# Kernel tuning notes

Measured on AMD Instinct MI355X. Metric: run time of the kernel, lower is better.

Reference implementation:

```python
import jax, jax.numpy as jnp
import numpy as np

NUM_BINS = 256
EPS = 1e-08


def setup_inputs() -> dict:
    key = jax.random.key(0)
    k1, k2 = jax.random.split(key)
    B, C, H, W = 16, 3, 512, 512
    pred = jax.random.uniform(k1, (B, C, H, W), dtype=jnp.float32)
    target = jax.random.uniform(k2, (B, C, H, W), dtype=jnp.float32)
    return {"pred": pred, "target": target}


def _compute_histogram(x):
    """Per-(batch, channel) 256-bin histogram of values in [0, 1].

    Faithful to torch.histc(bins=N, min=0, max=1): bin width 1/N,
    value v -> bin floor(v*N), with v == 1.0 landing in the last bin
    (handled by the clip). Values outside [0,1] are ignored.
    Implemented as a single fused scatter-add over all B*C histograms.
    """
    B, C, H, W = x.shape
    in_range = (x >= 0.0) & (x <= 1.0)
    bins = jnp.clip(jnp.floor(x * NUM_BINS).astype(jnp.int32), 0, NUM_BINS - 1)
    # flat index into [B*C, NUM_BINS] histogram array
    bc = jnp.arange(B * C, dtype=jnp.int32)[:, None]  # [B*C, 1]
    flat_idx = (bc * NUM_BINS + bins.reshape(B * C, H * W)).reshape(-1)
    weights = in_range.reshape(-1).astype(x.dtype)
    hist = jnp.zeros(B * C * NUM_BINS, dtype=x.dtype).at[flat_idx].add(weights)
    return hist.reshape(B, C, NUM_BINS)


def reference(pred, target):
    pred_hist = _compute_histogram(pred)
    target_hist = _compute_histogram(target)
    pred_hist = pred_hist / (pred_hist.sum(axis=2, keepdims=True) + EPS)
    target_hist = target_hist / (target_hist.sum(axis=2, keepdims=True) + EPS)
    return jnp.mean((pred_hist - target_hist) ** 2)
```

## Files before the change

kernel.cpp:

```cpp
#include <hip/hip_runtime.h>

#define NUM_BINS 256
#define PLANES 48
#define PLANE_ELEMS (512 * 512)
#define BPP 16
#define THREADS 256
#define F4_PER_BLOCK (PLANE_ELEMS / 4 / BPP)
#define F4_PER_THREAD (F4_PER_BLOCK / THREADS)
#define NSUB 8
#define HSTRIDE 257
#define BATCH 4

__global__ __launch_bounds__(THREADS) void hist_kernel(const float* __restrict__ pred,
                                                       const float* __restrict__ target,
                                                       unsigned* __restrict__ hist,
                                                       unsigned* __restrict__ totals) {
    __shared__ alignas(16) unsigned lh[NSUB * HSTRIDE];
    __shared__ unsigned twave[4];
    const int t = threadIdx.x;
    const int lane = t & 63;

    uint4* l4 = reinterpret_cast<uint4*>(lh);
    for (int i = t; i < (NSUB * HSTRIDE + 3) / 4; i += THREADS) l4[i] = make_uint4(0, 0, 0, 0);
    __syncthreads();

    const int gid   = blockIdx.x;
    const int which = gid / (PLANES * BPP);
    const int rem   = gid - which * (PLANES * BPP);
    const int plane = rem / BPP;
    const int cblk  = rem - plane * BPP;

    const float* src = which ? target : pred;
    const float4* p = reinterpret_cast<const float4*>(src + (size_t)plane * PLANE_ELEMS)
                      + (size_t)cblk * F4_PER_BLOCK;
    unsigned* gh = hist + (size_t)(which * PLANES + plane) * NUM_BINS;
    unsigned* tp = &totals[which * PLANES + plane];

    unsigned* sub = lh + (size_t)(lane & (NSUB - 1)) * HSTRIDE;

    float4 cur[BATCH], nxt[BATCH];
#pragma unroll
    for (int j = 0; j < BATCH; ++j) cur[j] = p[j * THREADS + t];

    for (int c = 0; c < F4_PER_THREAD / BATCH; ++c) {
        if (c + 1 < F4_PER_THREAD / BATCH) {
#pragma unroll
            for (int j = 0; j < BATCH; ++j)
                nxt[j] = p[(c + 1) * BATCH * THREADS + j * THREADS + t];
        }
#pragma unroll
        for (int j = 0; j < BATCH; ++j) {
            float e[4] = {cur[j].x, cur[j].y, cur[j].z, cur[j].w};
#pragma unroll
            for (int k = 0; k < 4; ++k) {
                int b = (int)(e[k] * 256.0f);
                b = b > 255 ? 255 : b;
                atomicAdd(&sub[b], 1u);
            }
        }
#pragma unroll
        for (int j = 0; j < BATCH; ++j) cur[j] = nxt[j];
    }
    __syncthreads();

    unsigned c = 0;
#pragma unroll
    for (int h = 0; h < NSUB; ++h) c += lh[h * HSTRIDE + t];
    if (c) atomicAdd(&gh[t], c);

    unsigned bt = c;
    for (int off = 32; off; off >>= 1) bt += __shfl_down(bt, off, 64);
    if ((t & 63) == 0) twave[t >> 6] = bt;
    __syncthreads();
    if (t == 0) atomicAdd(tp, twave[0] + twave[1] + twave[2] + twave[3]);
}

__global__ __launch_bounds__(1024) void loss_kernel(const unsigned* __restrict__ hist,
                                                    const unsigned* __restrict__ totals,
                                                    float* __restrict__ out) {
    __shared__ double inv[2 * PLANES];
    __shared__ double sd[16];
    const int t = threadIdx.x;
    if (t < 2 * PLANES) inv[t] = 1.0 / ((double)totals[t] + 1e-8);
    __syncthreads();

    const uint4* h4 = reinterpret_cast<const uint4*>(hist);
    double acc = 0.0;
    for (int i = t; i < (PLANES * NUM_BINS) / 4; i += 1024) {
        uint4 hp = h4[i];
        uint4 ht = h4[i + (PLANES * NUM_BINS) / 4];
        const double ip = inv[i >> 6];
        const double it = inv[PLANES + (i >> 6)];
        double d0 = (double)hp.x * ip - (double)ht.x * it;
        double d1 = (double)hp.y * ip - (double)ht.y * it;
        double d2 = (double)hp.z * ip - (double)ht.z * it;
        double d3 = (double)hp.w * ip - (double)ht.w * it;
        acc += d0 * d0 + d1 * d1 + d2 * d2 + d3 * d3;
    }
    for (int off = 32; off; off >>= 1) acc += __shfl_down(acc, off, 64);
    if ((t & 63) == 0) sd[t >> 6] = acc;
    __syncthreads();
    if (t == 0) {
        double s = 0.0;
        for (int w = 0; w < 16; ++w) s += sd[w];
        out[0] = (float)(s / (double)(PLANES * NUM_BINS));
    }
}

extern "C" void kernel_launch(void* const* d_in, const int* in_sizes, int n_in,
                              void* d_out, int out_size, void* d_ws, size_t ws_size,
                              hipStream_t stream) {
    const float* pred   = (const float*)d_in[0];
    const float* target = (const float*)d_in[1];
    float* out = (float*)d_out;
    unsigned* hist   = (unsigned*)d_ws;
    unsigned* totals = hist + (size_t)2 * PLANES * NUM_BINS;

    hipMemsetAsync(d_ws, 0, ((size_t)2 * PLANES * NUM_BINS + 2 * PLANES) * sizeof(unsigned), stream);
    hist_kernel<<<2 * PLANES * BPP, THREADS, 0, stream>>>(pred, target, hist, totals);
    loss_kernel<<<1, 1024, 0, stream>>>(hist, totals, out);
}
```

Baseline: 30.04 us.

## Replace global atomics and memset with per-block partial histograms and staged reductions

Each histogram block now writes its 256-bin partial histogram to its own workspace slot instead of atomically adding into shared global histograms and totals. This removes the memset launch and the global atomics. A per-plane kernel sums the 16 partials, computes the normalisation totals itself, and emits a per-plane loss, and a tiny final kernel reduces the 48 plane losses. The change trades the memset for one extra kernel launch and more workspace traffic for the partials.

```diff
diff --git a/kernel.cpp b/kernel.cpp
--- a/kernel.cpp
+++ b/kernel.cpp
@@ -13,10 +13,8 @@
 
 __global__ __launch_bounds__(THREADS) void hist_kernel(const float* __restrict__ pred,
                                                        const float* __restrict__ target,
-                                                       unsigned* __restrict__ hist,
-                                                       unsigned* __restrict__ totals) {
+                                                       unsigned* __restrict__ part) {
     __shared__ alignas(16) unsigned lh[NSUB * HSTRIDE];
-    __shared__ unsigned twave[4];
     const int t = threadIdx.x;
     const int lane = t & 63;
 
@@ -33,8 +31,6 @@
     const float* src = which ? target : pred;
     const float4* p = reinterpret_cast<const float4*>(src + (size_t)plane * PLANE_ELEMS)
                       + (size_t)cblk * F4_PER_BLOCK;
-    unsigned* gh = hist + (size_t)(which * PLANES + plane) * NUM_BINS;
-    unsigned* tp = &totals[which * PLANES + plane];
 
     unsigned* sub = lh + (size_t)(lane & (NSUB - 1)) * HSTRIDE;
 
@@ -66,45 +62,53 @@
     unsigned c = 0;
 #pragma unroll
     for (int h = 0; h < NSUB; ++h) c += lh[h * HSTRIDE + t];
-    if (c) atomicAdd(&gh[t], c);
-
-    unsigned bt = c;
-    for (int off = 32; off; off >>= 1) bt += __shfl_down(bt, off, 64);
-    if ((t & 63) == 0) twave[t >> 6] = bt;
-    __syncthreads();
-    if (t == 0) atomicAdd(tp, twave[0] + twave[1] + twave[2] + twave[3]);
+    part[(size_t)gid * NUM_BINS + t] = c;
 }
 
-__global__ __launch_bounds__(1024) void loss_kernel(const unsigned* __restrict__ hist,
-                                                    const unsigned* __restrict__ totals,
-                                                    float* __restrict__ out) {
-    __shared__ double inv[2 * PLANES];
-    __shared__ double sd[16];
+__global__ __launch_bounds__(THREADS) void plane_kernel(const unsigned* __restrict__ part,
+                                                        double* __restrict__ plane_loss) {
+    __shared__ unsigned wa[4], wb[4];
+    __shared__ double sd[THREADS];
     const int t = threadIdx.x;
-    if (t < 2 * PLANES) inv[t] = 1.0 / ((double)totals[t] + 1e-8);
+    const int p = blockIdx.x;
+
+    const unsigned* bp = part + (size_t)p * BPP * NUM_BINS;
+    const unsigned* bt = part + (size_t)(PLANES + p) * BPP * NUM_BINS;
+    unsigned hp = 0, ht = 0;
+#pragma unroll
+    for (int j = 0; j < BPP; ++j) {
+        hp += bp[j * NUM_BINS + t];
+        ht += bt[j * NUM_BINS + t];
+    }
+
+    unsigned a = hp, b = ht;
+    for (int off = 32; off; off >>= 1) {
+        a += __shfl_down(a, off, 64);
+        b += __shfl_down(b, off, 64);
+    }
+    if ((t & 63) == 0) { wa[t >> 6] = a; wb[t >> 6] = b; }
     __syncthreads();
+    const unsigned Sp = wa[0] + wa[1] + wa[2] + wa[3];
+    const unsigned St = wb[0] + wb[1] + wb[2] + wb[3];
 
-    const uint4* h4 = reinterpret_cast<const uint4*>(hist);
-    double acc = 0.0;
-    for (int i = t; i < (PLANES * NUM_BINS) / 4; i += 1024) {
-        uint4 hp = h4[i];
-        uint4 ht = h4[i + (PLANES * NUM_BINS) / 4];
-        const double ip = inv[i >> 6];
-        const double it = inv[PLANES + (i >> 6)];
-        double d0 = (double)hp.x * ip - (double)ht.x * it;
-        double d1 = (double)hp.y * ip - (double)ht.y * it;
-        double d2 = (double)hp.z * ip - (double)ht.z * it;
-        double d3 = (double)hp.w * ip - (double)ht.w * it;
-        acc += d0 * d0 + d1 * d1 + d2 * d2 + d3 * d3;
+    const double ip = 1.0 / ((double)Sp + 1e-8);
+    const double it = 1.0 / ((double)St + 1e-8);
+    const double d = (double)hp * ip - (double)ht * it;
+    sd[t] = d * d;
+    __syncthreads();
+    for (int off = THREADS / 2; off; off >>= 1) {
+        if (t < off) sd[t] += sd[t + off];
+        __syncthreads();
     }
-    for (int off = 32; off; off >>= 1) acc += __shfl_down(acc, off, 64);
-    if ((t & 63) == 0) sd[t >> 6] = acc;
-    __syncthreads();
-    if (t == 0) {
-        double s = 0.0;
-        for (int w = 0; w < 16; ++w) s += sd[w];
-        out[0] = (float)(s / (double)(PLANES * NUM_BINS));
-    }
+    if (t == 0) plane_loss[p] = sd[0];
+}
+
+__global__ __launch_bounds__(64) void final_kernel(const double* __restrict__ plane_loss,
+                                                   float* __restrict__ out) {
+    const int t = threadIdx.x;
+    double v = (t < PLANES) ? plane_loss[t] : 0.0;
+    for (int off = 32; off; off >>= 1) v += __shfl_down(v, off, 64);
+    if (t == 0) out[0] = (float)(v / (double)(PLANES * NUM_BINS));
 }
 
 extern "C" void kernel_launch(void* const* d_in, const int* in_sizes, int n_in,
@@ -113,10 +117,11 @@
     const float* pred   = (const float*)d_in[0];
     const float* target = (const float*)d_in[1];
     float* out = (float*)d_out;
-    unsigned* hist   = (unsigned*)d_ws;
-    unsigned* totals = hist + (size_t)2 * PLANES * NUM_BINS;
+    unsigned* part = (unsigned*)d_ws;
+    double* plane_loss = reinterpret_cast<double*>(
+        (char*)d_ws + (size_t)2 * PLANES * BPP * NUM_BINS * sizeof(unsigned));
 
-    hipMemsetAsync(d_ws, 0, ((size_t)2 * PLANES * NUM_BINS + 2 * PLANES) * sizeof(unsigned), stream);
-    hist_kernel<<<2 * PLANES * BPP, THREADS, 0, stream>>>(pred, target, hist, totals);
-    loss_kernel<<<1, 1024, 0, stream>>>(hist, totals, out);
+    hist_kernel<<<2 * PLANES * BPP, THREADS, 0, stream>>>(pred, target, part);
+    plane_kernel<<<PLANES, THREADS, 0, stream>>>(part, plane_loss);
+    final_kernel<<<1, 64, 0, stream>>>(plane_loss, out);
 }
```

Result: faster. 24.84 us, median of 2 (-17.3%).
